# Kernel tuning notes

Measured on AMD Instinct MI355X. Metric: run time of the kernel, lower is better.

The kernel has to match this reference:

```python
import jax, jax.numpy as jnp
import numpy as np

N = 50000   # nodes
E = 800000  # edges (before self loops)
F = 128     # in_dim
H = 4       # heads
C = 32      # hidden_dim per head
HC = H * C  # 128 == F
L = 3       # n_layers
G = 64      # graphs in batch
OUT = 64    # out_dim
NEG_SLOPE = 0.2


def setup_inputs() -> dict:
    key = jax.random.key(0)
    ks = jax.random.split(key, 12)
    s = 0.1
    x = jax.random.normal(ks[0], (N, F), jnp.float32)
    src = jax.random.randint(ks[1], (E,), 0, N, dtype=jnp.int32)
    dst = jax.random.randint(ks[2], (E,), 0, N, dtype=jnp.int32)
    # even split into G graphs so no graph is empty (segment_max safe)
    batch = (jnp.arange(N, dtype=jnp.int32) * G // N).astype(jnp.int32)
    Ws = jax.random.normal(ks[3], (L, HC, HC), jnp.float32) * s       # layer0 in=F=HC
    att_src = jax.random.normal(ks[4], (L, H, C), jnp.float32) * s
    att_dst = jax.random.normal(ks[5], (L, H, C), jnp.float32) * s
    conv_b = jnp.zeros((L, HC), jnp.float32)
    gate_W = jax.random.normal(ks[6], (L + 1, HC, 1), jnp.float32) * s
    gate_b = jnp.zeros((L + 1,), jnp.float32)
    lin_W = jax.random.normal(ks[7], (L + 1, HC, OUT), jnp.float32) * s
    lin_b = jnp.zeros((L + 1, OUT), jnp.float32)
    h_weights = jnp.ones((L + 1,), jnp.float32) / (L + 1)
    h0 = jax.random.normal(ks[8], (1,), jnp.float32)
    beta = jax.random.normal(ks[9], (OUT,), jnp.float32) * s
    pool_w = jnp.ones((3,), jnp.float32) / 3.0
    return dict(x=x, src=src, dst=dst, batch=batch, Ws=Ws, att_src=att_src,
                att_dst=att_dst, conv_b=conv_b, gate_W=gate_W, gate_b=gate_b,
                lin_W=lin_W, lin_b=lin_b, h_weights=h_weights, h0=h0,
                beta=beta, pool_w=pool_w)


def _seg_softmax(e, idx, n):
    # numerically stable softmax within segments
    m = jax.ops.segment_max(e, idx, num_segments=n)
    m = jnp.where(jnp.isfinite(m), m, 0.0)
    ex = jnp.exp(e - m[idx])
    s = jax.ops.segment_sum(ex, idx, num_segments=n)
    return ex / (s[idx] + 1e-16)


def _gat_layer(x, src, dst, W, a_src, a_dst, b):
    h = (x @ W).reshape(N, H, C)               # [N,H,C]
    al_s = jnp.sum(h * a_src, axis=-1)         # [N,H]
    al_d = jnp.sum(h * a_dst, axis=-1)         # [N,H]
    e = jax.nn.leaky_relu(al_s[src] + al_d[dst], NEG_SLOPE)  # [E+N,H]
    alpha = _seg_softmax(e, dst, N)            # softmax over incoming edges
    msg = h[src] * alpha[..., None]            # [E+N,H,C]
    out = jax.ops.segment_sum(msg, dst, num_segments=N)
    return out.reshape(N, HC) + b


def _pool_block(x, gw, gb, pool_w, batch, counts):
    gate = jax.nn.sigmoid(x @ gw + gb)[:, 0]          # [N]
    a = _seg_softmax(gate, batch, G)                  # per-graph attention
    p_att = jax.ops.segment_sum(a[:, None] * x, batch, num_segments=G)
    p_mean = jax.ops.segment_sum(x, batch, num_segments=G) / counts[:, None]
    p_max = jax.ops.segment_max(x, batch, num_segments=G)
    return pool_w[0] * p_att + pool_w[1] * p_mean + pool_w[2] * p_max


def reference(x, src, dst, batch, Ws, att_src, att_dst, conv_b, gate_W,
              gate_b, lin_W, lin_b, h_weights, h0, beta, pool_w):
    loops = jnp.arange(N, dtype=src.dtype)
    src_sl = jnp.concatenate([src, loops])
    dst_sl = jnp.concatenate([dst, loops])
    counts = jax.ops.segment_sum(jnp.ones((N,), x.dtype), batch, num_segments=G)
    out = jnp.zeros((G, OUT), x.dtype)
    for i in range(L):
        p = _pool_block(x, gate_W[i], gate_b[i], pool_w, batch, counts)
        out = out + h_weights[i] * (p @ lin_W[i] + lin_b[i])
        x = _gat_layer(x, src_sl, dst_sl, Ws[i], att_src[i], att_dst[i], conv_b[i])
        if i != L - 1:
            x = jax.nn.relu(x)
    p = _pool_block(x, gate_W[L], gate_b[L], pool_w, batch, counts)
    out = out + h_weights[L] * (p @ lin_W[L] + lin_b[L])
    risk_score = out @ beta + h0[0]   # [G]
    return risk_score
```

## Files before the change

kernel.cpp:

```cpp
#include <hip/hip_runtime.h>
#include <hip/hip_fp16.h>
#include <math.h>

#define N_NODES 50000
#define N_EDGES 800000
#define HC 128
#define NH 4
#define NG 64
#define NOUT 64
#define NLAYERS 3
#define POOL_CHUNKS 16
#define PREPW_BLOCKS (NLAYERS * HC * HC / 256)
#define NBKT ((N_NODES + 127) / 128)
#define PB_BLOCKS ((N_EDGES + 4095) / 4096)
#define GEMM_BLOCKS ((N_NODES + 15) / 16)
#define POOL2_BLOCKS (NG * POOL_CHUNKS / 2)
#define AGG_BLOCKS ((N_NODES + 3) / 4)
#define XT_STRIDE 136
#define ZREG_FLOATS ((NLAYERS + 1) * NG * HC * 2 + (NLAYERS + 1) * NG)
#define ZREG_BLOCKS ((ZREG_FLOATS / 4 + 255) / 256)
#define PMAX_BLOCKS ((NLAYERS + 1) * NG * HC / 4 / 256)
#define LOG2E 1.44269504f

typedef _Float16 v4h __attribute__((ext_vector_type(4)));
typedef float v4f __attribute__((ext_vector_type(4)));
typedef float v2f __attribute__((ext_vector_type(2)));

typedef unsigned char hh_t;

__device__ __forceinline__ void graph_range(int g, int* start, int* end) {
    *start = (int)(((long long)g * N_NODES + NG - 1) / NG);
    *end   = (int)(((long long)(g + 1) * N_NODES + NG - 1) / NG);
}

__device__ __forceinline__ float atomicMaxFloat(float* addr, float val) {
    if (val >= 0.f)
        return __int_as_float(atomicMax((int*)addr, __float_as_int(val)));
    else
        return __uint_as_float(atomicMin((unsigned int*)addr, __float_as_uint(val)));
}

__device__ __forceinline__ v2f hh_decode2(unsigned int packed) {
    return __builtin_amdgcn_cvt_pk_f32_fp8((int)packed, false);
}


template<bool F32>
__device__ __forceinline__ void gemm_body(
        int b, const void* xin, const _Float16* __restrict__ Wt,
        const float* __restrict__ a_src, const float* __restrict__ a_dst,
        hh_t* __restrict__ hh, float* __restrict__ al_s, float* __restrict__ al_d,
        __half* __restrict__ xh_out, const float* __restrict__ gw,
        const float* __restrict__ gbp, float* __restrict__ gate) {
    __shared__ __align__(16) _Float16 xt[16][XT_STRIDE];
    int t = threadIdx.x;
    int w = t >> 6;
    int l = t & 63;
    int n0 = b * 16;
    if constexpr (F32) {
        const float4* xg = (const float4*)((const float*)xin + (size_t)n0 * HC);
        float4 v0 = xg[t];
        float4 v1 = xg[t + 256];
        float4 gwv = ((const float4*)gw)[t & 31];
        float p0 = v0.x * gwv.x + v0.y * gwv.y + v0.z * gwv.z + v0.w * gwv.w;
        float p1 = v1.x * gwv.x + v1.y * gwv.y + v1.z * gwv.z + v1.w * gwv.w;
#pragma unroll
        for (int mk = 16; mk >= 1; mk >>= 1) {
            p0 += __shfl_xor(p0, mk);
            p1 += __shfl_xor(p1, mk);
        }
        if ((t & 31) == 0) {
            int r = t >> 5;
            float sg0 = 1.f / (1.f + __expf(-(p0 + gbp[0])));
            float sg1 = 1.f / (1.f + __expf(-(p1 + gbp[0])));
            gate[n0 + r]     = __expf(sg0);
            gate[n0 + 8 + r] = __expf(sg1);
        }
        __half2 h00 = __floats2half2_rn(v0.x, v0.y);
        __half2 h01 = __floats2half2_rn(v0.z, v0.w);
        __half2 h10 = __floats2half2_rn(v1.x, v1.y);
        __half2 h11 = __floats2half2_rn(v1.z, v1.w);
        uint2 pa, pb;
        pa.x = *(const uint*)&h00; pa.y = *(const uint*)&h01;
        pb.x = *(const uint*)&h10; pb.y = *(const uint*)&h11;
        int row = t >> 5, colh = (t & 31) * 4;
        *(uint2*)&xt[row][colh] = pa;
        *(uint2*)&xt[row + 8][colh] = pb;
        ((uint2*)xh_out)[(size_t)n0 * (HC / 4) + t]       = pa;
        ((uint2*)xh_out)[(size_t)n0 * (HC / 4) + t + 256] = pb;
    } else {
        uint4 v = ((const uint4*)((const __half*)xin + (size_t)n0 * HC))[t];
        *(uint4*)&xt[t >> 4][(t & 15) * 8] = v;
    }
    __syncthreads();
    int m = l & 15;
    int kg = (l >> 4) * 4;
    v4h a[8];
#pragma unroll
    for (int ks = 0; ks < 8; ks++)
        a[ks] = *(const v4h*)&xt[m][kg + ks * 16];
    __syncthreads();
    const _Float16* bp0 = Wt + (uint)(w * 32 + m) * HC + kg;
    const _Float16* bp1 = bp0 + 16 * HC;
    v4f acc0 = {0.f, 0.f, 0.f, 0.f}, acc1 = {0.f, 0.f, 0.f, 0.f};
#pragma unroll
    for (int ks = 0; ks < 8; ks++) {
        v4h b0 = *(const v4h*)(bp0 + ks * 16);
        v4h b1 = *(const v4h*)(bp1 + ks * 16);
        acc0 = __builtin_amdgcn_mfma_f32_16x16x16f16(a[ks], b0, acc0, 0, 0, 0);
        acc1 = __builtin_amdgcn_mfma_f32_16x16x16f16(a[ks], b1, acc1, 0, 0, 0);
    }
    int d0 = w * 32 + m;
    float as0 = a_src[d0] * LOG2E,      ad0 = a_dst[d0] * LOG2E;
    float as1 = a_src[d0 + 16] * LOG2E, ad1 = a_dst[d0 + 16] * LOG2E;
    int rloc = (l >> 4) * 4;
    unsigned char* xt8 = (unsigned char*)&xt[0][0];
#pragma unroll
    for (int r = 0; r < 4; r++) {
        int n = n0 + rloc + r;
        int q0 = __builtin_amdgcn_cvt_pk_fp8_f32(acc0[r], acc0[r], 0, false);
        int q1 = __builtin_amdgcn_cvt_pk_fp8_f32(acc1[r], acc1[r], 0, false);
        xt8[(rloc + r) * 136 + d0]      = (unsigned char)(q0 & 0xFF);
        xt8[(rloc + r) * 136 + d0 + 16] = (unsigned char)(q1 & 0xFF);
        float vs = acc0[r] * as0 + acc1[r] * as1;
        float vd = acc0[r] * ad0 + acc1[r] * ad1;
#pragma unroll
        for (int mk = 8; mk >= 1; mk >>= 1) {
            vs += __shfl_xor(vs, mk);
            vd += __shfl_xor(vd, mk);
        }
        if ((l & 15) == 0) {
            al_s[(uint)(n * NH + w)] = vs;
            al_d[(uint)(n * NH + w)] = vd;
        }
    }
    __syncthreads();
    uint2 v = *(const uint2*)&xt8[(t >> 4) * 136 + (t & 15) * 8];
    ((uint2*)hh)[(size_t)n0 * 16 + t] = v;
}

__device__ __forceinline__ void pool_body(
        int b, const __half* __restrict__ x, const float* __restrict__ gate,
        float* __restrict__ p_att, float* __restrict__ p_sum,
        float* __restrict__ p_max, float* __restrict__ wsum) {
    int c = b * 2 + (threadIdx.x >> 7);
    int g = c >> 4;
    int chunk = c & 15;
    int d = threadIdx.x & 127;
    int start, end; graph_range(g, &start, &end);
    int cnt = end - start;
    int cstart = start + (cnt * chunk) / POOL_CHUNKS;
    int cend   = start + (cnt * (chunk + 1)) / POOL_CHUNKS;
    float aat = 0.f, asu = 0.f, amx = -INFINITY, ws = 0.f;
    int n = cstart;
    for (; n + 4 <= cend; n += 4) {
        float w0 = gate[n],     w1 = gate[n + 1];
        float w2 = gate[n + 2], w3 = gate[n + 3];
        float x0 = __half2float(x[(uint)((n + 0) * HC + d)]);
        float x1 = __half2float(x[(uint)((n + 1) * HC + d)]);
        float x2 = __half2float(x[(uint)((n + 2) * HC + d)]);
        float x3 = __half2float(x[(uint)((n + 3) * HC + d)]);
        aat = fmaf(w0, x0, aat); aat = fmaf(w1, x1, aat);
        aat = fmaf(w2, x2, aat); aat = fmaf(w3, x3, aat);
        asu += (x0 + x1) + (x2 + x3);
        amx = fmaxf(amx, fmaxf(fmaxf(x0, x1), fmaxf(x2, x3)));
        ws += (w0 + w1) + (w2 + w3);
    }
    for (; n < cend; n++) {
        float w = gate[n];
        float xv = __half2float(x[(uint)(n * HC + d)]);
        aat = fmaf(w, xv, aat);
        asu += xv;
        amx = fmaxf(amx, xv);
        ws += w;
    }
    atomicAdd(&p_att[g * HC + d], aat);
    atomicAdd(&p_sum[g * HC + d], asu);
    atomicMaxFloat(&p_max[g * HC + d], amx);
    if (d == 0) atomicAdd(&wsum[g], ws);
}

__device__ __forceinline__ void scat2_body(
        int bkt, const int* __restrict__ part, const int* __restrict__ bktbase,
        int* __restrict__ rowptr, int* __restrict__ csr_src) {
    __shared__ int degs[128];
    __shared__ int curs[128];
    __shared__ int w0tot;
    int t = threadIdx.x;
    int nstart = bkt << 7;
    int nend = nstart + 128; if (nend > N_NODES) nend = N_NODES;
    int nloc = nend - nstart;
    int estart = bktbase[bkt], eend = bktbase[bkt + 1];
    if (t < 128) degs[t] = 0;
    __syncthreads();
    for (int e = estart + t; e < eend; e += 256)
        atomicAdd(&degs[(part[e] >> 16) & 127], 1);
    __syncthreads();
    int v = 0, inc = 0;
    if (t < 128) {
        v = degs[t];
        inc = v;
#pragma unroll
        for (int off = 1; off < 64; off <<= 1) {
            int u = __shfl_up(inc, off);
            if ((t & 63) >= off) inc += u;
        }
    }
    if (t == 63) w0tot = inc;
    __syncthreads();
    if (t < 128) {
        int excl = inc - v + ((t >= 64) ? w0tot : 0);
        int rp = estart + excl;
        curs[t] = rp;
        if (t < nloc) rowptr[nstart + t] = rp;
    }
    __syncthreads();
    for (int e = estart + t; e < eend; e += 256) {
        int p = part[e];
        int pos = atomicAdd(&curs[(p >> 16) & 127], 1);
        csr_src[pos] = p & 0xFFFF;
    }
}

__device__ __forceinline__ void agg_body(
        int b, const hh_t* __restrict__ hh, const float* __restrict__ al_s,
        const float* __restrict__ al_d, const int* __restrict__ rowptr,
        const int* __restrict__ csr_src, const float* __restrict__ conv_b,
        __half* __restrict__ xout, int do_relu,
        const float* __restrict__ gw, const float* __restrict__ gbp,
        float* __restrict__ gate) {
    int n = b * 4 + (threadIdx.x >> 6);
    if (n >= N_NODES) return;
    int l = threadIdx.x & 63;
    int head = l >> 4;
    int le = l & 15;
    float ad = al_d[(uint)(n * NH + head)];
    const unsigned short* hhp = (const unsigned short*)hh;
    float e0 = al_s[(uint)(n * NH + head)] + ad;
    e0 = fmaxf(e0, 0.2f * e0);
    float s_uni = exp2f(e0);
    v2f vself = hh_decode2(hhp[(uint)(n * 64 + l)]);
    float ax = s_uni * vself[0], ay = s_uni * vself[1];
    int jb = rowptr[n], je = rowptr[n + 1];
    float s_part = 0.f;
    for (int j = jb; j < je; j += 16) {
        int rem = je - j;
        bool act = le < rem;
        int my_s = csr_src[j + (act ? le : 0)];
        float aa = al_s[(uint)(my_s * NH + head)];
        float e = aa + ad;
        e = fmaxf(e, 0.2f * e);
        float ex = act ? exp2f(e) : 0.f;
        s_part += ex;
        int exb = __float_as_int(ex);
        unsigned int vv[16];
#pragma unroll
        for (int u = 0; u < 16; u++) {
            int ssu = __builtin_amdgcn_readlane(my_s, u);
            vv[u] = hhp[((size_t)(uint)ssu << 6) + l];
        }
#define AGG_SLOT(U) {                                                        \
            float exu = __int_as_float(                                      \
                __builtin_amdgcn_ds_swizzle(exb, 16 + 32 * (U)));            \
            v2f vf = hh_decode2(vv[U]);                                      \
            ax = fmaf(exu, vf[0], ax);                                       \
            ay = fmaf(exu, vf[1], ay);                                       \
        }
        AGG_SLOT(0)  AGG_SLOT(1)  AGG_SLOT(2)  AGG_SLOT(3)
        AGG_SLOT(4)  AGG_SLOT(5)  AGG_SLOT(6)  AGG_SLOT(7)
        AGG_SLOT(8)  AGG_SLOT(9)  AGG_SLOT(10) AGG_SLOT(11)
        AGG_SLOT(12) AGG_SLOT(13) AGG_SLOT(14) AGG_SLOT(15)
#undef AGG_SLOT
    }
    s_part += __shfl_xor(s_part, 1);
    s_part += __shfl_xor(s_part, 2);
    s_part += __shfl_xor(s_part, 4);
    s_part += __shfl_xor(s_part, 8);
    float s = s_part + s_uni;
    float inv = 1.f / (s + 1e-16f);
    float2 cb = ((const float2*)conv_b)[l];
    float r0 = fmaf(ax, inv, cb.x);
    float r1 = fmaf(ay, inv, cb.y);
    if (do_relu) { r0 = fmaxf(r0, 0.f); r1 = fmaxf(r1, 0.f); }
    ((__half2*)xout)[(uint)(n * 64 + l)] = __floats2half2_rn(r0, r1);
    float2 gwv = ((const float2*)gw)[l];
    float gv = r0 * gwv.x + r1 * gwv.y;
#pragma unroll
    for (int m = 32; m >= 1; m >>= 1) gv += __shfl_xor(gv, m);
    if (l == 0) {
        float sg = 1.f / (1.f + __expf(-(gv + gbp[0])));
        gate[n] = __expf(sg);
    }
}


__global__ __launch_bounds__(256) void k_prep(
        const float* __restrict__ Ws, _Float16* __restrict__ Wt,
        const int* __restrict__ dst, int* __restrict__ bh,
        float* __restrict__ zreg, uint* __restrict__ pmaxw) {
    int b = blockIdx.x;
    int t = threadIdx.x;
    if (b < PREPW_BLOCKS) {
        int e = b * 256 + t;
        int layer = e >> 14; int r = e & 16383; int k = r >> 7; int d = r & 127;
        Wt[layer * 16384 + d * 128 + k] = (_Float16)Ws[layer * 16384 + k * 128 + d];
    } else if (b < PREPW_BLOCKS + PB_BLOCKS) {
        int pb = b - PREPW_BLOCKS;
        __shared__ int cnt[NBKT];
        for (int i = t; i < NBKT; i += 256) cnt[i] = 0;
        __syncthreads();
        int base = pb * 4096;
#pragma unroll
        for (int k = 0; k < 16; k++) {
            int e = base + t + 256 * k;
            if (e < N_EDGES) atomicAdd(&cnt[dst[e] >> 7], 1);
        }
        __syncthreads();
        for (int i = t; i < NBKT; i += 256) bh[i * PB_BLOCKS + pb] = cnt[i];
    } else {
        int zb = b - PREPW_BLOCKS - PB_BLOCKS;
        if (zb < ZREG_BLOCKS) {
            int i = zb * 256 + t;
            if (i < ZREG_FLOATS / 4)
                ((float4*)zreg)[i] = make_float4(0.f, 0.f, 0.f, 0.f);
        } else {
            int i = (zb - ZREG_BLOCKS) * 256 + t;
            uint4 f; f.x = f.y = f.z = f.w = 0xFFFFFFFFu;
            ((uint4*)pmaxw)[i] = f;
        }
    }
}

__global__ __launch_bounds__(256) void k_scan_bh(int* __restrict__ bh,
                                                 int* __restrict__ bkttot) {
    __shared__ int tmp[256];
    int bkt = blockIdx.x, t = threadIdx.x;
    int v = (t < PB_BLOCKS) ? bh[bkt * PB_BLOCKS + t] : 0;
    tmp[t] = v;
    __syncthreads();
    for (int off = 1; off < 256; off <<= 1) {
        int u = (t >= off) ? tmp[t - off] : 0;
        __syncthreads();
        tmp[t] += u;
        __syncthreads();
    }
    if (t < PB_BLOCKS) bh[bkt * PB_BLOCKS + t] = tmp[t] - v;
    if (t == 255) bkttot[bkt] = tmp[255];
}

__global__ __launch_bounds__(512) void k_bktbase(const int* __restrict__ bkttot,
                                                 int* __restrict__ bktbase,
                                                 int* __restrict__ rowptr) {
    __shared__ int tmp[512];
    int t = threadIdx.x;
    int v = (t < NBKT) ? bkttot[t] : 0;
    tmp[t] = v;
    __syncthreads();
    for (int off = 1; off < 512; off <<= 1) {
        int u = (t >= off) ? tmp[t - off] : 0;
        __syncthreads();
        tmp[t] += u;
        __syncthreads();
    }
    if (t < NBKT) bktbase[t] = tmp[t] - v;
    if (t == NBKT - 1) {
        bktbase[NBKT] = tmp[t];
        rowptr[N_NODES] = tmp[t];
    }
}

__global__ __launch_bounds__(256) void k_part(
        const int* __restrict__ src, const int* __restrict__ dst,
        const int* __restrict__ bktbase, const int* __restrict__ bh,
        int* __restrict__ part) {
    __shared__ int curs[NBKT];
    int blk = blockIdx.x, t = threadIdx.x;
    for (int i = t; i < NBKT; i += 256)
        curs[i] = bktbase[i] + bh[i * PB_BLOCKS + blk];
    __syncthreads();
    int base = blk * 4096;
#pragma unroll
    for (int k = 0; k < 16; k++) {
        int e = base + t + 256 * k;
        if (e < N_EDGES) {
            int d = dst[e];
            int pos = atomicAdd(&curs[d >> 7], 1);
            part[pos] = src[e] | ((d & 127) << 16);
        }
    }
}


__global__ __launch_bounds__(256) void k_fused_a2(
        const int* __restrict__ part, const int* __restrict__ bktbase,
        int* __restrict__ rowptr, int* __restrict__ csr_src,
        const float* __restrict__ x0, const _Float16* __restrict__ Wt,
        const float* __restrict__ a_src, const float* __restrict__ a_dst,
        hh_t* __restrict__ hh, float* __restrict__ al_s, float* __restrict__ al_d,
        __half* __restrict__ x0h, const float* __restrict__ gw,
        const float* __restrict__ gbp, float* __restrict__ gate) {
    int b = blockIdx.x;
    if (b < NBKT) {
        scat2_body(b, part, bktbase, rowptr, csr_src);
    } else {
        gemm_body<true>(b - NBKT, x0, Wt, a_src, a_dst, hh, al_s, al_d,
                        x0h, gw, gbp, gate);
    }
}

__global__ __launch_bounds__(256) void k_fused_agg(
        const hh_t* __restrict__ hh, const float* __restrict__ al_s,
        const float* __restrict__ al_d, const int* __restrict__ rowptr,
        const int* __restrict__ csr_src, const float* __restrict__ conv_b,
        __half* __restrict__ xout, int do_relu,
        const float* __restrict__ gw, const float* __restrict__ gbp,
        float* __restrict__ gate_out,
        const __half* __restrict__ xp, const float* __restrict__ gate_in,
        float* __restrict__ p_att, float* __restrict__ p_sum,
        float* __restrict__ p_max, float* __restrict__ wsum) {
    int b = blockIdx.x;
    if (b < POOL2_BLOCKS) {
        pool_body(b, xp, gate_in, p_att, p_sum, p_max, wsum);
    } else {
        agg_body(b - POOL2_BLOCKS, hh, al_s, al_d, rowptr, csr_src, conv_b,
                 xout, do_relu, gw, gbp, gate_out);
    }
}

__global__ __launch_bounds__(256) void k_fused_b(
        const __half* __restrict__ x, const _Float16* __restrict__ Wt,
        const float* __restrict__ a_src, const float* __restrict__ a_dst,
        hh_t* __restrict__ hh, float* __restrict__ al_s, float* __restrict__ al_d,
        const float* __restrict__ gate,
        float* __restrict__ p_att, float* __restrict__ p_sum,
        float* __restrict__ p_max, float* __restrict__ wsum) {
    int b = blockIdx.x;
    if (b < GEMM_BLOCKS) {
        gemm_body<false>(b, x, Wt, a_src, a_dst, hh, al_s, al_d,
                         nullptr, nullptr, nullptr, nullptr);
    } else {
        pool_body(b - GEMM_BLOCKS, x, gate, p_att, p_sum, p_max, wsum);
    }
}

__global__ __launch_bounds__(256) void k_agg(
        const hh_t* __restrict__ hh, const float* __restrict__ al_s,
        const float* __restrict__ al_d, const int* __restrict__ rowptr,
        const int* __restrict__ csr_src, const float* __restrict__ conv_b,
        __half* __restrict__ xout, int do_relu,
        const float* __restrict__ gw, const float* __restrict__ gbp,
        float* __restrict__ gate) {
    agg_body(blockIdx.x, hh, al_s, al_d, rowptr, csr_src, conv_b,
             xout, do_relu, gw, gbp, gate);
}

__global__ __launch_bounds__(256) void k_pool(
        const __half* __restrict__ x, const float* __restrict__ gate,
        float* __restrict__ p_att, float* __restrict__ p_sum,
        float* __restrict__ p_max, float* __restrict__ wsum) {
    pool_body(blockIdx.x, x, gate, p_att, p_sum, p_max, wsum);
}


__global__ __launch_bounds__(128) void k_finish(
        const float* __restrict__ p_att, const float* __restrict__ p_sum,
        const float* __restrict__ p_max, const float* __restrict__ wsum,
        const float* __restrict__ pool_w, const float* __restrict__ lin_W,
        const float* __restrict__ lin_b, const float* __restrict__ hw,
        const float* __restrict__ beta, const float* __restrict__ h0,
        float* __restrict__ out) {
    int g = blockIdx.x, t = threadIdx.x;
    __shared__ float p[NLAYERS + 1][HC];
    int start, end; graph_range(g, &start, &end);
    float cinv = 1.f / (float)(end - start);
    float pw0 = pool_w[0], pw1 = pool_w[1], pw2 = pool_w[2];
#pragma unroll
    for (int j = 0; j <= NLAYERS; j++) {
        float winv = 1.f / (wsum[j * NG + g] + 1e-16f);
        p[j][t] = pw0 * p_att[(j * NG + g) * HC + t] * winv
                + pw1 * p_sum[(j * NG + g) * HC + t] * cinv
                + pw2 * p_max[(j * NG + g) * HC + t];
    }
    __syncthreads();
    if (t < NOUT) {
        float acc = 0.f;
#pragma unroll
        for (int j = 0; j <= NLAYERS; j++) {
            float a = lin_b[j * NOUT + t];
            const float* Wj = lin_W + (size_t)j * HC * NOUT;
            for (int k = 0; k < HC; k++) a = fmaf(p[j][k], Wj[k * NOUT + t], a);
            acc = fmaf(hw[j], a, acc);
        }
        float v = acc * beta[t];
#pragma unroll
        for (int m = 32; m >= 1; m >>= 1) v += __shfl_xor(v, m);
        if (t == 0) out[g] = v + h0[0];
    }
}


extern "C" void kernel_launch(void* const* d_in, const int* in_sizes, int n_in,
                              void* d_out, int out_size, void* d_ws, size_t ws_size,
                              hipStream_t stream) {
    const float* x0       = (const float*)d_in[0];
    const int*   src      = (const int*)d_in[1];
    const int*   dst      = (const int*)d_in[2];
    const float* Ws       = (const float*)d_in[4];
    const float* att_src  = (const float*)d_in[5];
    const float* att_dst  = (const float*)d_in[6];
    const float* conv_b   = (const float*)d_in[7];
    const float* gate_W   = (const float*)d_in[8];
    const float* gate_b   = (const float*)d_in[9];
    const float* lin_W    = (const float*)d_in[10];
    const float* lin_b    = (const float*)d_in[11];
    const float* h_w      = (const float*)d_in[12];
    const float* h0       = (const float*)d_in[13];
    const float* beta     = (const float*)d_in[14];
    const float* pool_w   = (const float*)d_in[15];

    char* base = (char*)d_ws;
    size_t off = 0;
    auto carve = [&](size_t bytes) -> char* {
        char* p = base + off;
        off = (off + bytes + 255) & ~(size_t)255;
        return p;
    };
    __half*    x0h     = (__half*)carve((size_t)N_NODES * HC * 2);
    __half*    xA      = (__half*)carve((size_t)N_NODES * HC * 2);
    __half*    xB      = (__half*)carve((size_t)N_NODES * HC * 2);
    hh_t*      hh      = (hh_t*)carve((size_t)N_NODES * HC);
    _Float16*  Wt      = (_Float16*)carve((size_t)NLAYERS * HC * HC * 2);
    float*     al_s    = (float*)carve((size_t)N_NODES * NH * 4);
    float*     al_d    = (float*)carve((size_t)N_NODES * NH * 4);
    float*     gateA   = (float*)carve((size_t)N_NODES * 4);
    float*     gateB   = (float*)carve((size_t)N_NODES * 4);
    int*       rowptr  = (int*)carve((size_t)(N_NODES + 1) * 4);
    int*       csrsrc  = (int*)carve((size_t)N_EDGES * 4);
    int*       bh      = (int*)carve((size_t)NBKT * PB_BLOCKS * 4);
    int*       bkttot  = (int*)carve((size_t)NBKT * 4);
    int*       bktbase = (int*)carve((size_t)(NBKT + 1) * 4);
    int*       part    = (int*)carve((size_t)N_EDGES * 4);
    float*     zreg    = (float*)carve((size_t)ZREG_FLOATS * 4);
    float*     p_att   = zreg;
    float*     p_sum   = zreg + (size_t)(NLAYERS + 1) * NG * HC;
    float*     wsum    = p_sum + (size_t)(NLAYERS + 1) * NG * HC;
    float*     p_max   = (float*)carve((size_t)(NLAYERS + 1) * NG * HC * 4);

    k_prep<<<PREPW_BLOCKS + PB_BLOCKS + ZREG_BLOCKS + PMAX_BLOCKS, 256, 0, stream>>>(
        Ws, Wt, dst, bh, zreg, (uint*)p_max);

    k_scan_bh<<<NBKT, 256, 0, stream>>>(bh, bkttot);
    k_bktbase<<<1, 512, 0, stream>>>(bkttot, bktbase, rowptr);
    k_part<<<PB_BLOCKS, 256, 0, stream>>>(src, dst, bktbase, bh, part);

    k_fused_a2<<<NBKT + GEMM_BLOCKS, 256, 0, stream>>>(
        part, bktbase, rowptr, csrsrc,
        x0, Wt, att_src, att_dst, hh, al_s, al_d,
        x0h, gate_W, gate_b, gateA);

    k_fused_agg<<<POOL2_BLOCKS + AGG_BLOCKS, 256, 0, stream>>>(
        hh, al_s, al_d, rowptr, csrsrc, conv_b,
        xA, 1, gate_W + HC, gate_b + 1, gateB,
        x0h, gateA, p_att, p_sum, p_max, wsum);

    k_fused_b<<<GEMM_BLOCKS + POOL2_BLOCKS, 256, 0, stream>>>(
        xA, Wt + (size_t)1 * HC * HC, att_src + HC, att_dst + HC,
        hh, al_s, al_d, gateB,
        p_att + (size_t)1 * NG * HC, p_sum + (size_t)1 * NG * HC,
        p_max + (size_t)1 * NG * HC, wsum + 1 * NG);

    k_agg<<<AGG_BLOCKS, 256, 0, stream>>>(
        hh, al_s, al_d, rowptr, csrsrc, conv_b + HC,
        xB, 1, gate_W + 2 * HC, gate_b + 2, gateA);

    k_fused_b<<<GEMM_BLOCKS + POOL2_BLOCKS, 256, 0, stream>>>(
        xB, Wt + (size_t)2 * HC * HC, att_src + 2 * HC, att_dst + 2 * HC,
        hh, al_s, al_d, gateA,
        p_att + (size_t)2 * NG * HC, p_sum + (size_t)2 * NG * HC,
        p_max + (size_t)2 * NG * HC, wsum + 2 * NG);

    k_agg<<<AGG_BLOCKS, 256, 0, stream>>>(
        hh, al_s, al_d, rowptr, csrsrc, conv_b + 2 * HC,
        xA, 0, gate_W + 3 * HC, gate_b + 3, gateB);

    k_pool<<<POOL2_BLOCKS, 256, 0, stream>>>(
        xA, gateB,
        p_att + (size_t)3 * NG * HC, p_sum + (size_t)3 * NG * HC,
        p_max + (size_t)3 * NG * HC, wsum + 3 * NG);

    k_finish<<<NG, 128, 0, stream>>>(p_att, p_sum, p_max, wsum, pool_w,
                                     lin_W, lin_b, h_w, beta, h0, (float*)d_out);
}
```

Measured before the change: 245.8 us.

## Drop bucket-base scan kernel and co-schedule pooling with aggregation instead of GEMM

Removes the single-block k_bktbase launch. Each consumer now derives bucket offsets from bkttot itself: k_part runs a 512-wide shared-memory scan, and each scatter block does a block reduction over the preceding buckets. rowptr[N] is written in k_prep instead. For layers 2 and 3, graph pooling moves out of the GEMM kernel and into the fused aggregation kernel, so the GEMM runs alone. The aim is less launch and serialization overhead and better load balance, paid for with redundant per-block scan work.

```diff
diff --git a/kernel.cpp b/kernel.cpp
--- a/kernel.cpp
+++ b/kernel.cpp
@@ -181,16 +181,27 @@
 }
 
 __device__ __forceinline__ void scat2_body(
-        int bkt, const int* __restrict__ part, const int* __restrict__ bktbase,
+        int bkt, const int* __restrict__ part, const int* __restrict__ bkttot,
         int* __restrict__ rowptr, int* __restrict__ csr_src) {
     __shared__ int degs[128];
     __shared__ int curs[128];
+    __shared__ int red[256];
     __shared__ int w0tot;
     int t = threadIdx.x;
+    int a = 0;
+    for (int i = t; i < NBKT; i += 256)
+        if (i < bkt) a += bkttot[i];
+    red[t] = a;
+    __syncthreads();
+    for (int o = 128; o > 0; o >>= 1) {
+        if (t < o) red[t] += red[t + o];
+        __syncthreads();
+    }
+    int estart = red[0];
+    int eend = estart + bkttot[bkt];
     int nstart = bkt << 7;
     int nend = nstart + 128; if (nend > N_NODES) nend = N_NODES;
     int nloc = nend - nstart;
-    int estart = bktbase[bkt], eend = bktbase[bkt + 1];
     if (t < 128) degs[t] = 0;
     __syncthreads();
     for (int e = estart + t; e < eend; e += 256)
@@ -297,9 +308,11 @@
 __global__ __launch_bounds__(256) void k_prep(
         const float* __restrict__ Ws, _Float16* __restrict__ Wt,
         const int* __restrict__ dst, int* __restrict__ bh,
-        float* __restrict__ zreg, uint* __restrict__ pmaxw) {
+        float* __restrict__ zreg, uint* __restrict__ pmaxw,
+        int* __restrict__ rowptr) {
     int b = blockIdx.x;
     int t = threadIdx.x;
+    if (b == 0 && t == 0) rowptr[N_NODES] = N_EDGES;
     if (b < PREPW_BLOCKS) {
         int e = b * 256 + t;
         int layer = e >> 14; int r = e & 16383; int k = r >> 7; int d = r & 127;
@@ -348,35 +361,26 @@
     if (t == 255) bkttot[bkt] = tmp[255];
 }
 
-__global__ __launch_bounds__(512) void k_bktbase(const int* __restrict__ bkttot,
-                                                 int* __restrict__ bktbase,
-                                                 int* __restrict__ rowptr) {
-    __shared__ int tmp[512];
-    int t = threadIdx.x;
-    int v = (t < NBKT) ? bkttot[t] : 0;
-    tmp[t] = v;
-    __syncthreads();
-    for (int off = 1; off < 512; off <<= 1) {
-        int u = (t >= off) ? tmp[t - off] : 0;
-        __syncthreads();
-        tmp[t] += u;
-        __syncthreads();
-    }
-    if (t < NBKT) bktbase[t] = tmp[t] - v;
-    if (t == NBKT - 1) {
-        bktbase[NBKT] = tmp[t];
-        rowptr[N_NODES] = tmp[t];
-    }
-}
-
 __global__ __launch_bounds__(256) void k_part(
         const int* __restrict__ src, const int* __restrict__ dst,
-        const int* __restrict__ bktbase, const int* __restrict__ bh,
+        const int* __restrict__ bkttot, const int* __restrict__ bh,
         int* __restrict__ part) {
     __shared__ int curs[NBKT];
+    __shared__ int scan[512];
     int blk = blockIdx.x, t = threadIdx.x;
+    scan[t]       = (t < NBKT) ? bkttot[t] : 0;
+    scan[t + 256] = (t + 256 < NBKT) ? bkttot[t + 256] : 0;
+    __syncthreads();
+    for (int off = 1; off < 512; off <<= 1) {
+        int u0 = (t >= off) ? scan[t - off] : 0;
+        int u1 = scan[t + 256 - off];
+        __syncthreads();
+        scan[t] += u0;
+        scan[t + 256] += u1;
+        __syncthreads();
+    }
     for (int i = t; i < NBKT; i += 256)
-        curs[i] = bktbase[i] + bh[i * PB_BLOCKS + blk];
+        curs[i] = (i ? scan[i - 1] : 0) + bh[i * PB_BLOCKS + blk];
     __syncthreads();
     int base = blk * 4096;
 #pragma unroll
@@ -392,7 +396,7 @@
 
 
 __global__ __launch_bounds__(256) void k_fused_a2(
-        const int* __restrict__ part, const int* __restrict__ bktbase,
+        const int* __restrict__ part, const int* __restrict__ bkttot,
         int* __restrict__ rowptr, int* __restrict__ csr_src,
         const float* __restrict__ x0, const _Float16* __restrict__ Wt,
         const float* __restrict__ a_src, const float* __restrict__ a_dst,
@@ -401,7 +405,7 @@
         const float* __restrict__ gbp, float* __restrict__ gate) {
     int b = blockIdx.x;
     if (b < NBKT) {
-        scat2_body(b, part, bktbase, rowptr, csr_src);
+        scat2_body(b, part, bkttot, rowptr, csr_src);
     } else {
         gemm_body<true>(b - NBKT, x0, Wt, a_src, a_dst, hh, al_s, al_d,
                         x0h, gw, gbp, gate);
@@ -427,31 +431,12 @@
     }
 }
 
-__global__ __launch_bounds__(256) void k_fused_b(
+__global__ __launch_bounds__(256) void k_gemm(
         const __half* __restrict__ x, const _Float16* __restrict__ Wt,
         const float* __restrict__ a_src, const float* __restrict__ a_dst,
-        hh_t* __restrict__ hh, float* __restrict__ al_s, float* __restrict__ al_d,
-        const float* __restrict__ gate,
-        float* __restrict__ p_att, float* __restrict__ p_sum,
-        float* __restrict__ p_max, float* __restrict__ wsum) {
-    int b = blockIdx.x;
-    if (b < GEMM_BLOCKS) {
-        gemm_body<false>(b, x, Wt, a_src, a_dst, hh, al_s, al_d,
-                         nullptr, nullptr, nullptr, nullptr);
-    } else {
-        pool_body(b - GEMM_BLOCKS, x, gate, p_att, p_sum, p_max, wsum);
-    }
-}
-
-__global__ __launch_bounds__(256) void k_agg(
-        const hh_t* __restrict__ hh, const float* __restrict__ al_s,
-        const float* __restrict__ al_d, const int* __restrict__ rowptr,
-        const int* __restrict__ csr_src, const float* __restrict__ conv_b,
-        __half* __restrict__ xout, int do_relu,
-        const float* __restrict__ gw, const float* __restrict__ gbp,
-        float* __restrict__ gate) {
-    agg_body(blockIdx.x, hh, al_s, al_d, rowptr, csr_src, conv_b,
-             xout, do_relu, gw, gbp, gate);
+        hh_t* __restrict__ hh, float* __restrict__ al_s, float* __restrict__ al_d) {
+    gemm_body<false>(blockIdx.x, x, Wt, a_src, a_dst, hh, al_s, al_d,
+                     nullptr, nullptr, nullptr, nullptr);
 }
 
 __global__ __launch_bounds__(256) void k_pool(
@@ -538,7 +523,6 @@
     int*       csrsrc  = (int*)carve((size_t)N_EDGES * 4);
     int*       bh      = (int*)carve((size_t)NBKT * PB_BLOCKS * 4);
     int*       bkttot  = (int*)carve((size_t)NBKT * 4);
-    int*       bktbase = (int*)carve((size_t)(NBKT + 1) * 4);
     int*       part    = (int*)carve((size_t)N_EDGES * 4);
     float*     zreg    = (float*)carve((size_t)ZREG_FLOATS * 4);
     float*     p_att   = zreg;
@@ -547,14 +531,13 @@
     float*     p_max   = (float*)carve((size_t)(NLAYERS + 1) * NG * HC * 4);
 
     k_prep<<<PREPW_BLOCKS + PB_BLOCKS + ZREG_BLOCKS + PMAX_BLOCKS, 256, 0, stream>>>(
-        Ws, Wt, dst, bh, zreg, (uint*)p_max);
+        Ws, Wt, dst, bh, zreg, (uint*)p_max, rowptr);
 
     k_scan_bh<<<NBKT, 256, 0, stream>>>(bh, bkttot);
-    k_bktbase<<<1, 512, 0, stream>>>(bkttot, bktbase, rowptr);
-    k_part<<<PB_BLOCKS, 256, 0, stream>>>(src, dst, bktbase, bh, part);
+    k_part<<<PB_BLOCKS, 256, 0, stream>>>(src, dst, bkttot, bh, part);
 
     k_fused_a2<<<NBKT + GEMM_BLOCKS, 256, 0, stream>>>(
-        part, bktbase, rowptr, csrsrc,
+        part, bkttot, rowptr, csrsrc,
         x0, Wt, att_src, att_dst, hh, al_s, al_d,
         x0h, gate_W, gate_b, gateA);
 
@@ -563,25 +546,27 @@
         xA, 1, gate_W + HC, gate_b + 1, gateB,
         x0h, gateA, p_att, p_sum, p_max, wsum);
 
-    k_fused_b<<<GEMM_BLOCKS + POOL2_BLOCKS, 256, 0, stream>>>(
+    k_gemm<<<GEMM_BLOCKS, 256, 0, stream>>>(
         xA, Wt + (size_t)1 * HC * HC, att_src + HC, att_dst + HC,
-        hh, al_s, al_d, gateB,
+        hh, al_s, al_d);
+
+    k_fused_agg<<<POOL2_BLOCKS + AGG_BLOCKS, 256, 0, stream>>>(
+        hh, al_s, al_d, rowptr, csrsrc, conv_b + HC,
+        xB, 1, gate_W + 2 * HC, gate_b + 2, gateA,
+        xA, gateB,
         p_att + (size_t)1 * NG * HC, p_sum + (size_t)1 * NG * HC,
         p_max + (size_t)1 * NG * HC, wsum + 1 * NG);
 
-    k_agg<<<AGG_BLOCKS, 256, 0, stream>>>(
-        hh, al_s, al_d, rowptr, csrsrc, conv_b + HC,
-        xB, 1, gate_W + 2 * HC, gate_b + 2, gateA);
-
-    k_fused_b<<<GEMM_BLOCKS + POOL2_BLOCKS, 256, 0, stream>>>(
+    k_gemm<<<GEMM_BLOCKS, 256, 0, stream>>>(
         xB, Wt + (size_t)2 * HC * HC, att_src + 2 * HC, att_dst + 2 * HC,
-        hh, al_s, al_d, gateA,
+        hh, al_s, al_d);
+
+    k_fused_agg<<<POOL2_BLOCKS + AGG_BLOCKS, 256, 0, stream>>>(
+        hh, al_s, al_d, rowptr, csrsrc, conv_b + 2 * HC,
+        xA, 0, gate_W + 3 * HC, gate_b + 3, gateB,
+        xB, gateA,
         p_att + (size_t)2 * NG * HC, p_sum + (size_t)2 * NG * HC,
         p_max + (size_t)2 * NG * HC, wsum + 2 * NG);
-
-    k_agg<<<AGG_BLOCKS, 256, 0, stream>>>(
-        hh, al_s, al_d, rowptr, csrsrc, conv_b + 2 * HC,
-        xA, 0, gate_W + 3 * HC, gate_b + 3, gateB);
 
     k_pool<<<POOL2_BLOCKS, 256, 0, stream>>>(
         xA, gateB,
```

After: 252.6 us. 1.03x slower.
